# Optimization experiments

Hardware: AMD Instinct MI355X
Metric: run time of the kernel (lower is better)

## Reference

```python
import jax, jax.numpy as jnp
import numpy as np

R = 16            # grid resolution
WIN = 8           # window size (voxels per side)
NW3 = (R // WIN) ** 3   # number of windows = 8
WS = WIN ** 3           # tokens per window = 512
N = R ** 3              # active voxels = 4096
C = 512; H = 8; DH = C // H; L = 8; LAT = 8
NG = 4; VOX = 0.015625; OUTC = 14 * NG; MLP = 4 * C


def _radical_inverse(base, i):
    f = 1.0; r = 0.0
    while i > 0:
        f /= base; r += f * (i % base); i //= base
    return r


def _offset_perturbation():
    # hammersley_sequence(3, i, NG) = [i/NG, phi_2(i), phi_3(i)]
    p = np.array([[i / NG, _radical_inverse(2, i), _radical_inverse(3, i)] for i in range(NG)], np.float32)
    p = p * 2.0 - 1.0
    p = np.clip(p / VOX, -0.99, 0.99)
    return jnp.asarray(np.arctanh(p).astype(np.float32))  # [NG, 3]


def setup_inputs() -> dict:
    key = jax.random.key(0)
    ks = jax.random.split(key, 12)
    nw = R // WIN
    # window-major voxel ordering: dense 16^3 grid grouped into 8^3 windows
    win = np.stack(np.meshgrid(*[np.arange(nw)] * 3, indexing='ij'), -1).reshape(-1, 3)
    inner = np.stack(np.meshgrid(*[np.arange(WIN)] * 3, indexing='ij'), -1).reshape(-1, 3)
    xyz = (win[:, None, :] * WIN + inner[None, :, :]).reshape(-1, 3).astype(np.int32)
    coords = jnp.asarray(np.concatenate([np.zeros((N, 1), np.int32), xyz], axis=1))  # [N,4] (batch,x,y,z)
    s = 0.02
    return {
        'feats': jax.random.normal(ks[0], (N, LAT), jnp.float32),
        'coords': coords,
        'emb_x': jax.random.normal(ks[1], (1024, C // 3), jnp.float32) * s,
        'emb_y': jax.random.normal(ks[2], (1024, C // 3), jnp.float32) * s,
        'emb_z': jax.random.normal(ks[3], (1024, C - 2 * (C // 3)), jnp.float32) * s,
        'w_in': jax.random.normal(ks[4], (LAT, C), jnp.float32) * s,
        'b_in': jnp.zeros((C,), jnp.float32),
        'ln1_g': jnp.ones((L, C), jnp.float32), 'ln1_b': jnp.zeros((L, C), jnp.float32),
        'w_qkv': jax.random.normal(ks[5], (L, C, 3 * C), jnp.float32) * s,
        'b_qkv': jnp.zeros((L, 3 * C), jnp.float32),
        'w_o': jax.random.normal(ks[6], (L, C, C), jnp.float32) * s,
        'b_o': jnp.zeros((L, C), jnp.float32),
        'ln2_g': jnp.ones((L, C), jnp.float32), 'ln2_b': jnp.zeros((L, C), jnp.float32),
        'w_m1': jax.random.normal(ks[7], (L, C, MLP), jnp.float32) * s,
        'b_m1': jnp.zeros((L, MLP), jnp.float32),
        'w_m2': jax.random.normal(ks[8], (L, MLP, C), jnp.float32) * s,
        'b_m2': jnp.zeros((L, C), jnp.float32),
        'w_out': jax.random.normal(ks[9], (C, OUTC), jnp.float32) * s,
        'b_out': jnp.zeros((OUTC,), jnp.float32),
        'offset_perturb': _offset_perturbation(),
    }


def _ln(x, g, b, eps):
    m = jnp.mean(x, axis=-1, keepdims=True)
    v = jnp.var(x, axis=-1, keepdims=True)
    return (x - m) * jax.lax.rsqrt(v + eps) * g + b


def _forward(feats, coords, emb_x, emb_y, emb_z, w_in, b_in, ln1_g, ln1_b,
             w_qkv, b_qkv, w_o, b_o, ln2_g, ln2_b, w_m1, b_m1, w_m2, b_m2,
             w_out, b_out, offset_perturb):
    # input_layer + absolute position embedding (gather from 3 tables)
    h = feats @ w_in + b_in  # [N, C]
    pe = jnp.concatenate([emb_x[coords[:, 1]], emb_y[coords[:, 2]], emb_z[coords[:, 3]]], axis=-1)
    h = h + pe

    def block(h, p):
        l1g, l1b, wq, bq, wo, bo, l2g, l2b, w1, b1, w2, b2 = p
        a = _ln(h, l1g, l1b, 1e-6)
        qkv = (a @ wq + bq).reshape(NW3, WS, 3, H, DH)  # voxels are window-major
        q, k, v = qkv[:, :, 0], qkv[:, :, 1], qkv[:, :, 2]
        scores = jnp.einsum('wqhd,wkhd->whqk', q, k) / jnp.sqrt(jnp.float32(DH))
        attn = jax.nn.softmax(scores, axis=-1)
        o = jnp.einsum('whqk,wkhd->wqhd', attn, v).reshape(N, C)
        h = h + o @ wo + bo
        m = _ln(h, l2g, l2b, 1e-6)
        h = h + jax.nn.gelu(m @ w1 + b1) @ w2 + b2
        return h, None

    params = (ln1_g, ln1_b, w_qkv, b_qkv, w_o, b_o, ln2_g, ln2_b, w_m1, b_m1, w_m2, b_m2)
    h, _ = jax.lax.scan(block, h, params)

    # final non-affine layer_norm + out projection
    h = _ln(h, jnp.ones((C,), h.dtype), jnp.zeros((C,), h.dtype), 1e-5)
    out = h @ w_out + b_out  # [N, 56]

    # to_representation (single batch)
    xyz_base = (coords[:, 1:].astype(jnp.float32) + 0.5) / R  # [N, 3]
    off = out[:, 0:3 * NG].reshape(N, NG, 3) + offset_perturb
    off = jnp.tanh(off) / R * 0.5 * VOX
    _xyz = (xyz_base[:, None, :] + off).reshape(N * NG, 3)
    _fdc = out[:, 3 * NG:6 * NG].reshape(N * NG, 1, 3)
    _scal = out[:, 6 * NG:9 * NG].reshape(N * NG, 3)
    _rot = out[:, 9 * NG:13 * NG].reshape(N * NG, 4)
    _opa = out[:, 13 * NG:14 * NG].reshape(N * NG, 1)
    return _xyz, _fdc, _scal, _rot, _opa


def reference(feats, coords, emb_x, emb_y, emb_z, w_in, b_in, ln1_g, ln1_b,
              w_qkv, b_qkv, w_o, b_o, ln2_g, ln2_b, w_m1, b_m1, w_m2, b_m2,
              w_out, b_out, offset_perturb):
    return _forward(feats, coords, emb_x, emb_y, emb_z, w_in, b_in, ln1_g, ln1_b,
                    w_qkv, b_qkv, w_o, b_o, ln2_g, ln2_b, w_m1, b_m1, w_m2, b_m2,
                    w_out, b_out, offset_perturb)
```

## Files before the change

kernel.cpp:

```cpp
#include <hip/hip_runtime.h>
#include <stdint.h>

typedef unsigned short u16;
typedef short bf16x8 __attribute__((ext_vector_type(8)));
typedef float f32x4 __attribute__((ext_vector_type(4)));

#define NTOK 4096
#define CDIM 512
#define NHEAD 8
#define LAYERS 8
#define MLPD 2048
#define QKVD 1536

__device__ __forceinline__ u16 f2bf(float f){
  union { float f; unsigned u; } c; c.f = f;
  return (u16)((c.u + 0x7FFFu + ((c.u >> 16) & 1u)) >> 16);
}

__device__ __forceinline__ unsigned pack2(float a, float b){
  return (unsigned)f2bf(a) | ((unsigned)f2bf(b) << 16);
}

__device__ __forceinline__ void llds16(const void* g, void* l){
  __builtin_amdgcn_global_load_lds((const __attribute__((address_space(1))) void*)g,
                                   (__attribute__((address_space(3))) void*)l, 16, 0, 0);
}

template<int N> __device__ __forceinline__ void wait_vmcnt(){
  if constexpr (N == 0) asm volatile("s_waitcnt vmcnt(0)" ::: "memory");
  else if constexpr (N == 2) asm volatile("s_waitcnt vmcnt(2)" ::: "memory");
  else if constexpr (N == 4) asm volatile("s_waitcnt vmcnt(4)" ::: "memory");
  else static_assert(N == 0 || N == 2 || N == 4, "unsupported vmcnt");
}

__global__ void kt_transpose(const float* __restrict__ W, u16* __restrict__ Wt, int K, int N){
  __shared__ float tile[32][33];
  int l = blockIdx.z;
  W  += (size_t)l * K * N;
  Wt += (size_t)l * K * N;
  int k0 = blockIdx.y * 32, n0 = blockIdx.x * 32;
  int t = threadIdx.x;
  int r = t >> 3, c4 = (t & 7) << 2;
  float4 v = *(const float4*)&W[(size_t)(k0 + r) * N + n0 + c4];
  tile[r][c4 + 0] = v.x; tile[r][c4 + 1] = v.y; tile[r][c4 + 2] = v.z; tile[r][c4 + 3] = v.w;
  __syncthreads();
  ushort4 o;
  o.x = f2bf(tile[c4 + 0][r]);
  o.y = f2bf(tile[c4 + 1][r]);
  o.z = f2bf(tile[c4 + 2][r]);
  o.w = f2bf(tile[c4 + 3][r]);
  *(ushort4*)&Wt[(size_t)(n0 + r) * K + k0 + c4] = o;
}

__global__ void kt_embed(const float* __restrict__ feats, const int* __restrict__ coords,
                         const float* __restrict__ ex, const float* __restrict__ ey,
                         const float* __restrict__ ez, const float* __restrict__ w_in,
                         const float* __restrict__ b_in, float* __restrict__ h){
  __shared__ float fs[8];
  __shared__ int cc[3];
  int n = blockIdx.x, t = threadIdx.x;
  if (t < 8) fs[t] = feats[n * 8 + t];
  if (t == 8) { cc[0] = coords[n*4+1]; cc[1] = coords[n*4+2]; cc[2] = coords[n*4+3]; }
  __syncthreads();
  for (int c = t; c < CDIM; c += 256){
    float acc = b_in[c];
    #pragma unroll
    for (int i = 0; i < 8; i++) acc += fs[i] * w_in[i * CDIM + c];
    float pe;
    if (c < 170)      pe = ex[cc[0] * 170 + c];
    else if (c < 340) pe = ey[cc[1] * 170 + (c - 170)];
    else              pe = ez[cc[2] * 172 + (c - 340)];
    h[(size_t)n * CDIM + c] = acc + pe;
  }
}

__global__ void kt_ln(const float* __restrict__ h, const float* __restrict__ g,
                      const float* __restrict__ b, u16* __restrict__ out, float eps){
  int wave = threadIdx.x >> 6, lane = threadIdx.x & 63;
  int row = blockIdx.x * 4 + wave;
  const float* hr = h + (size_t)row * CDIM + lane * 8;
  float4 v0 = *(const float4*)hr, v1 = *(const float4*)(hr + 4);
  float x[8] = {v0.x, v0.y, v0.z, v0.w, v1.x, v1.y, v1.z, v1.w};
  float s = 0.f, q = 0.f;
  #pragma unroll
  for (int i = 0; i < 8; i++){ s += x[i]; q += x[i] * x[i]; }
  #pragma unroll
  for (int off = 32; off; off >>= 1){ s += __shfl_xor(s, off); q += __shfl_xor(q, off); }
  float mean = s * (1.0f / CDIM);
  float var  = q * (1.0f / CDIM) - mean * mean;
  float rr = rsqrtf(var + eps);
  int cb = lane * 8;
  u16 u[8];
  #pragma unroll
  for (int i = 0; i < 8; i++)
    u[i] = f2bf((x[i] - mean) * rr * g[cb + i] + b[cb + i]);
  uint4 pk;
  pk.x = (unsigned)u[0] | ((unsigned)u[1] << 16);
  pk.y = (unsigned)u[2] | ((unsigned)u[3] << 16);
  pk.z = (unsigned)u[4] | ((unsigned)u[5] << 16);
  pk.w = (unsigned)u[6] | ((unsigned)u[7] << 16);
  *(uint4*)&out[(size_t)row * CDIM + cb] = pk;
}

template<int BM, int BN, int MODE>
__global__ __launch_bounds__(256) void kt_gemm(
    const u16* __restrict__ A, const u16* __restrict__ Wt, const float* __restrict__ bias,
    u16* __restrict__ outb, float* __restrict__ hres, u16* __restrict__ vT, int N, int K)
{
  constexpr int MF = BM / 32;
  constexpr int NF = BN / 32;
  constexpr int Mt = NTOK / BM;
  constexpr int Mx = Mt / 8;
  __shared__ __align__(16) u16 As[2][BM * 64];
  __shared__ __align__(16) u16 Bs[2][BN * 64];
  int tid = threadIdx.x, wave = tid >> 6, lane = tid & 63;

  int Nt = N / BN;
  int bid = blockIdx.x;
  int xcd = bid & 7, slot = bid >> 3;
  int miL = slot / Nt;
  int ni = slot - miL * Nt;
  int m0 = (xcd * Mx + miL) * BM, n0 = ni * BN;

  int wm = wave >> 1, wn = wave & 1;
  f32x4 acc[MF][NF];
  const f32x4 fzero = {0.f, 0.f, 0.f, 0.f};
  #pragma unroll
  for (int m = 0; m < MF; m++)
    #pragma unroll
    for (int n = 0; n < NF; n++) acc[m][n] = fzero;

  int srow = lane >> 3;
  int sblk = (lane & 7) ^ srow;
  const u16* gA = A  + (size_t)(m0 + wave * 8 + srow) * K + sblk * 8;
  const u16* gB = Wt + (size_t)(n0 + wave * 8 + srow) * K + sblk * 8;

  auto stage = [&](int buf, int kt){
    #pragma unroll
    for (int j = 0; j < MF; j++)
      llds16(gA + (size_t)(j * 32) * K + kt, &As[buf][(j * 32 + wave * 8) * 64]);
    #pragma unroll
    for (int j = 0; j < NF; j++)
      llds16(gB + (size_t)(j * 32) * K + kt, &Bs[buf][(j * 32 + wave * 8) * 64]);
  };

  int nk = K >> 6;
  stage(0, 0);
  __syncthreads();
  int rl = lane & 15, hg = lane >> 4;
  for (int t = 0; t < nk; ++t){
    int cur = t & 1;
    if (t + 1 < nk) stage(cur ^ 1, (t + 1) << 6);
    #pragma unroll
    for (int kk = 0; kk < 2; kk++){
      bf16x8 af[MF], bfr[NF];
      int bl = (kk << 2) + hg;
      #pragma unroll
      for (int m = 0; m < MF; m++){
        int row = wm * (BM / 2) + m * 16 + rl;
        af[m] = *(const bf16x8*)&As[cur][row * 64 + ((bl ^ (row & 7)) << 3)];
      }
      #pragma unroll
      for (int n = 0; n < NF; n++){
        int row = wn * (BN / 2) + n * 16 + rl;
        bfr[n] = *(const bf16x8*)&Bs[cur][row * 64 + ((bl ^ (row & 7)) << 3)];
      }
      #pragma unroll
      for (int m = 0; m < MF; m++)
        #pragma unroll
        for (int n = 0; n < NF; n++)
          acc[m][n] = __builtin_amdgcn_mfma_f32_16x16x32_bf16(af[m], bfr[n], acc[m][n], 0, 0, 0);
    }
    __syncthreads();
  }

  int cl = lane & 15, rg = lane >> 4;
  #pragma unroll
  for (int m = 0; m < MF; m++){
    int row0 = m0 + wm * (BM / 2) + m * 16 + rg * 4;
    #pragma unroll
    for (int n = 0; n < NF; n++){
      int col = n0 + wn * (BN / 2) + n * 16 + cl;
      float bb = bias[col];
      if (MODE == 1){
        #pragma unroll
        for (int r = 0; r < 4; r++){
          size_t idx = (size_t)(row0 + r) * N + col;
          hres[idx] += acc[m][n][r] + bb;
        }
      } else if (MODE == 2){
        #pragma unroll
        for (int r = 0; r < 4; r++){
          float x = acc[m][n][r] + bb;
          float t = 0.7978845608028654f * (x + 0.044715f * x * x * x);
          float sg = 1.0f / (1.0f + __expf(-2.0f * t));
          outb[(size_t)(row0 + r) * N + col] = f2bf(x * sg);
        }
      } else {
        if (col < 1024){
          #pragma unroll
          for (int r = 0; r < 4; r++)
            outb[(size_t)(row0 + r) * N + col] = f2bf(acc[m][n][r] + bb);
        } else {
          int dh = col - 1024;
          int win = row0 >> 9, tin = row0 & 511;
          ushort4 p;
          p.x = f2bf(acc[m][n][0] + bb);
          p.y = f2bf(acc[m][n][1] + bb);
          p.z = f2bf(acc[m][n][2] + bb);
          p.w = f2bf(acc[m][n][3] + bb);
          *(ushort4*)&vT[(size_t)(win * 512 + dh) * 512 + tin] = p;
        }
      }
    }
  }
}

__global__ __launch_bounds__(256) void kt_attn(const u16* __restrict__ qkv,
                                               const u16* __restrict__ vT,
                                               u16* __restrict__ o){
  __shared__ __align__(16) u16 Ks[3][32 * 64];
  __shared__ __align__(16) u16 Vs[3][64 * 32];
  int tid = threadIdx.x, wave = tid >> 6, lane = tid & 63;
  int bx = blockIdx.x;
  int win = bx >> 6, head = (bx >> 3) & 7, q8 = bx & 7;
  int rl = lane & 15, hg = lane >> 4;
  int qbase = win * 512 + q8 * 64 + wave * 16;
  const u16* qptr  = qkv + (size_t)(qbase + rl) * QKVD + head * 64;
  const u16* kbase = qkv + (size_t)(win * 512) * QKVD + 512 + head * 64;
  const u16* vbase = vT + (size_t)(win * 512 + head * 64) * 512;

  int krow = tid >> 3;
  const u16* gK = kbase + (size_t)krow * QKVD + (((tid & 7) ^ (krow & 7)) << 3);
  int vrow = tid >> 2;
  const u16* gV = vbase + (size_t)vrow * 512 + (((tid & 3) ^ (vrow & 3)) << 3);

  auto stage = [&](int buf, int kt){
    llds16(gK + (size_t)kt * QKVD, &Ks[buf][tid * 8]);
    llds16(gV + kt, &Vs[buf][tid * 8]);
  };

  bf16x8 qf0 = *(const bf16x8*)(qptr + hg * 8);
  bf16x8 qf1 = *(const bf16x8*)(qptr + 32 + hg * 8);

  const f32x4 fzero = {0.f, 0.f, 0.f, 0.f};
  f32x4 Oa[4] = {fzero, fzero, fzero, fzero};
  float mrun = -1e30f, lrun = 0.f;

  stage(0, 0);
  stage(1, 32);
  for (int t = 0; t < 16; ++t){
    int cur = t % 3;
    if (t + 1 < 16) wait_vmcnt<2>(); else wait_vmcnt<0>();
    __builtin_amdgcn_s_barrier();
    asm volatile("" ::: "memory");
    if (t + 2 < 16) stage((t + 2) % 3, (t + 2) * 32);

    bf16x8 kf[2][2];
    #pragma unroll
    for (int c = 0; c < 2; c++)
      #pragma unroll
      for (int dk = 0; dk < 2; dk++){
        int row = c * 16 + rl;
        kf[c][dk] = *(const bf16x8*)&Ks[cur][row * 64 + ((((dk << 2) + hg) ^ (rl & 7)) << 3)];
      }
    bf16x8 vf[4];
    #pragma unroll
    for (int d = 0; d < 4; d++){
      int row = d * 16 + rl;
      vf[d] = *(const bf16x8*)&Vs[cur][row * 32 + ((hg ^ (rl & 3)) << 3)];
    }

    f32x4 s0 = fzero, s1 = fzero;
    s0 = __builtin_amdgcn_mfma_f32_16x16x32_bf16(kf[0][0], qf0, s0, 0, 0, 0);
    s0 = __builtin_amdgcn_mfma_f32_16x16x32_bf16(kf[0][1], qf1, s0, 0, 0, 0);
    s1 = __builtin_amdgcn_mfma_f32_16x16x32_bf16(kf[1][0], qf0, s1, 0, 0, 0);
    s1 = __builtin_amdgcn_mfma_f32_16x16x32_bf16(kf[1][1], qf1, s1, 0, 0, 0);
    float v[8];
    #pragma unroll
    for (int r = 0; r < 4; r++){ v[r] = s0[r] * 0.125f; v[4 + r] = s1[r] * 0.125f; }
    float tmax = v[0];
    #pragma unroll
    for (int i = 1; i < 8; i++) tmax = fmaxf(tmax, v[i]);
    tmax = fmaxf(tmax, __shfl_xor(tmax, 16));
    tmax = fmaxf(tmax, __shfl_xor(tmax, 32));
    float mnew = fmaxf(mrun, tmax);
    float corr = __expf(mrun - mnew);
    mrun = mnew;
    float p[8], ps = 0.f;
    #pragma unroll
    for (int i = 0; i < 8; i++){ p[i] = __expf(v[i] - mnew); ps += p[i]; }
    ps += __shfl_xor(ps, 16);
    ps += __shfl_xor(ps, 32);
    lrun = lrun * corr + ps;
    float c0 = __shfl(corr, (hg << 2) + 0);
    float c1 = __shfl(corr, (hg << 2) + 1);
    float c2 = __shfl(corr, (hg << 2) + 2);
    float c3 = __shfl(corr, (hg << 2) + 3);
    #pragma unroll
    for (int d = 0; d < 4; d++){
      Oa[d][0] *= c0; Oa[d][1] *= c1; Oa[d][2] *= c2; Oa[d][3] *= c3;
    }
    unsigned pk00 = pack2(p[0], p[1]);
    unsigned pk01 = pack2(p[2], p[3]);
    unsigned pk10 = pack2(p[4], p[5]);
    unsigned pk11 = pack2(p[6], p[7]);
    int idx0 = rl | ((( hg << 1)      & 3) << 4);
    int idx1 = rl | ((((hg << 1) + 1) & 3) << 4);
    bool hiC = hg >= 2;
    unsigned W0a = __shfl(pk00, idx0), W0b = __shfl(pk10, idx0);
    unsigned W1a = __shfl(pk01, idx0), W1b = __shfl(pk11, idx0);
    unsigned W2a = __shfl(pk00, idx1), W2b = __shfl(pk10, idx1);
    unsigned W3a = __shfl(pk01, idx1), W3b = __shfl(pk11, idx1);
    uint4 W;
    W.x = hiC ? W0b : W0a;
    W.y = hiC ? W1b : W1a;
    W.z = hiC ? W2b : W2a;
    W.w = hiC ? W3b : W3a;
    bf16x8 pf;
    __builtin_memcpy(&pf, &W, 16);
    #pragma unroll
    for (int d = 0; d < 4; d++)
      Oa[d] = __builtin_amdgcn_mfma_f32_16x16x32_bf16(pf, vf[d], Oa[d], 0, 0, 0);
  }

  float l0 = __shfl(lrun, (hg << 2) + 0);
  float l1 = __shfl(lrun, (hg << 2) + 1);
  float l2 = __shfl(lrun, (hg << 2) + 2);
  float l3 = __shfl(lrun, (hg << 2) + 3);
  float li[4] = {1.f / l0, 1.f / l1, 1.f / l2, 1.f / l3};
  #pragma unroll
  for (int d = 0; d < 4; d++)
    #pragma unroll
    for (int r = 0; r < 4; r++){
      int row = qbase + (hg << 2) + r;
      o[(size_t)row * CDIM + head * 64 + d * 16 + rl] = f2bf(Oa[d][r] * li[r]);
    }
}

__global__ void kt_final(const float* __restrict__ h, const float* __restrict__ w_out,
                         const float* __restrict__ b_out, const int* __restrict__ coords,
                         const float* __restrict__ offp, float* __restrict__ out){
  __shared__ float lnv[CDIM];
  __shared__ float ov[56];
  int n = blockIdx.x, lane = threadIdx.x;
  const float* hr = h + (size_t)n * CDIM + lane * 8;
  float4 v0 = *(const float4*)hr, v1 = *(const float4*)(hr + 4);
  float x[8] = {v0.x, v0.y, v0.z, v0.w, v1.x, v1.y, v1.z, v1.w};
  float s = 0.f, q = 0.f;
  #pragma unroll
  for (int i = 0; i < 8; i++){ s += x[i]; q += x[i] * x[i]; }
  #pragma unroll
  for (int off = 32; off; off >>= 1){ s += __shfl_xor(s, off); q += __shfl_xor(q, off); }
  float mean = s * (1.0f / CDIM);
  float var  = q * (1.0f / CDIM) - mean * mean;
  float rr = rsqrtf(var + 1e-5f);
  #pragma unroll
  for (int i = 0; i < 8; i++) lnv[lane * 8 + i] = (x[i] - mean) * rr;
  __syncthreads();
  if (lane < 56){
    float a = b_out[lane];
    for (int k = 0; k < CDIM; k++) a += lnv[k] * w_out[k * 56 + lane];
    ov[lane] = a;
  }
  __syncthreads();
  if (lane < 12){
    int g = lane / 3, d = lane - g * 3;
    float base = ((float)coords[n * 4 + 1 + d] + 0.5f) * (1.0f / 16.0f);
    float t = tanhf(ov[lane] + offp[lane]);
    out[(size_t)n * 12 + lane] = base + t * 4.8828125e-4f;
    out[49152  + (size_t)n * 12 + lane] = ov[12 + lane];
    out[98304  + (size_t)n * 12 + lane] = ov[24 + lane];
  }
  if (lane < 16) out[147456 + (size_t)n * 16 + lane] = ov[36 + lane];
  if (lane < 4)  out[212992 + (size_t)n * 4  + lane] = ov[52 + lane];
}

extern "C" void kernel_launch(void* const* d_in, const int* in_sizes, int n_in,
                              void* d_out, int out_size, void* d_ws, size_t ws_size,
                              hipStream_t stream) {
  const float* feats = (const float*)d_in[0];
  const int*   coords = (const int*)d_in[1];
  const float* emb_x = (const float*)d_in[2];
  const float* emb_y = (const float*)d_in[3];
  const float* emb_z = (const float*)d_in[4];
  const float* w_in  = (const float*)d_in[5];
  const float* b_in  = (const float*)d_in[6];
  const float* ln1_g = (const float*)d_in[7];
  const float* ln1_b = (const float*)d_in[8];
  const float* w_qkv = (const float*)d_in[9];
  const float* b_qkv = (const float*)d_in[10];
  const float* w_o   = (const float*)d_in[11];
  const float* b_o   = (const float*)d_in[12];
  const float* ln2_g = (const float*)d_in[13];
  const float* ln2_b = (const float*)d_in[14];
  const float* w_m1  = (const float*)d_in[15];
  const float* b_m1  = (const float*)d_in[16];
  const float* w_m2  = (const float*)d_in[17];
  const float* b_m2  = (const float*)d_in[18];
  const float* w_out = (const float*)d_in[19];
  const float* b_out = (const float*)d_in[20];
  const float* offp  = (const float*)d_in[21];

  char* ws = (char*)d_ws;
  auto carve = [&](size_t bytes){ char* p = ws; ws += (bytes + 255) & ~(size_t)255; return p; };
  float* h   = (float*)carve((size_t)NTOK * CDIM * 4);
  u16* a     = (u16*)carve((size_t)NTOK * CDIM * 2);
  u16* qkvb  = (u16*)carve((size_t)NTOK * QKVD * 2);
  u16* vT    = (u16*)carve((size_t)NTOK * CDIM * 2);
  u16* ob    = (u16*)carve((size_t)NTOK * CDIM * 2);
  u16* ub    = (u16*)carve((size_t)NTOK * MLPD * 2);
  u16* wqkvT = (u16*)carve((size_t)LAYERS * QKVD * CDIM * 2);
  u16* woT   = (u16*)carve((size_t)LAYERS * CDIM * CDIM * 2);
  u16* wm1T  = (u16*)carve((size_t)LAYERS * MLPD * CDIM * 2);
  u16* wm2T  = (u16*)carve((size_t)LAYERS * CDIM * MLPD * 2);

  kt_transpose<<<dim3(QKVD/32, CDIM/32, LAYERS), 256, 0, stream>>>(w_qkv, wqkvT, CDIM, QKVD);
  kt_transpose<<<dim3(CDIM/32, CDIM/32, LAYERS), 256, 0, stream>>>(w_o,   woT,   CDIM, CDIM);
  kt_transpose<<<dim3(MLPD/32, CDIM/32, LAYERS), 256, 0, stream>>>(w_m1,  wm1T,  CDIM, MLPD);
  kt_transpose<<<dim3(CDIM/32, MLPD/32, LAYERS), 256, 0, stream>>>(w_m2,  wm2T,  MLPD, CDIM);
  kt_embed<<<NTOK, 256, 0, stream>>>(feats, coords, emb_x, emb_y, emb_z, w_in, b_in, h);

  for (int l = 0; l < LAYERS; ++l){
    kt_ln<<<NTOK/4, 256, 0, stream>>>(h, ln1_g + l*CDIM, ln1_b + l*CDIM, a, 1e-6f);
    kt_gemm<128,128,0><<<(NTOK/128)*(QKVD/128), 256, 0, stream>>>(
        a, wqkvT + (size_t)l*QKVD*CDIM, b_qkv + l*QKVD, qkvb, nullptr, vT, QKVD, CDIM);
    kt_attn<<<512, 256, 0, stream>>>(qkvb, vT, ob);
    kt_gemm<64,64,1><<<(NTOK/64)*(CDIM/64), 256, 0, stream>>>(
        ob, woT + (size_t)l*CDIM*CDIM, b_o + l*CDIM, nullptr, h, nullptr, CDIM, CDIM);
    kt_ln<<<NTOK/4, 256, 0, stream>>>(h, ln2_g + l*CDIM, ln2_b + l*CDIM, a, 1e-6f);
    kt_gemm<128,128,2><<<(NTOK/128)*(MLPD/128), 256, 0, stream>>>(
        a, wm1T + (size_t)l*MLPD*CDIM, b_m1 + l*MLPD, ub, nullptr, nullptr, MLPD, CDIM);
    kt_gemm<64,64,1><<<(NTOK/64)*(CDIM/64), 256, 0, stream>>>(
        ub, wm2T + (size_t)l*CDIM*MLPD, b_m2 + l*CDIM, nullptr, h, nullptr, CDIM, MLPD);
  }
  kt_final<<<NTOK, 64, 0, stream>>>(h, w_out, b_out, coords, offp, (float*)d_out);
}
```

Baseline: 855.2 us.

## Fuse LayerNorm into QKV and MLP1 GEMM A-operand loading

Removes the standalone LayerNorm kernels and instead has the QKV and MLP-up GEMMs read fp32 residual rows directly. Each block first computes per-row mean and rstd into shared memory, then normalizes, converts to bf16 and writes swizzled A tiles into LDS in register-staged double buffering. This drops two launches per layer and the bf16 activation round trip through global memory. In exchange, every N-tile block recomputes row statistics and reads fp32 A (twice the bytes of bf16), which is redundant work across the 12 or 16 column tiles.

```diff
diff --git a/kernel.cpp b/kernel.cpp
--- a/kernel.cpp
+++ b/kernel.cpp
@@ -74,37 +74,11 @@
   }
 }
 
-__global__ void kt_ln(const float* __restrict__ h, const float* __restrict__ g,
-                      const float* __restrict__ b, u16* __restrict__ out, float eps){
-  int wave = threadIdx.x >> 6, lane = threadIdx.x & 63;
-  int row = blockIdx.x * 4 + wave;
-  const float* hr = h + (size_t)row * CDIM + lane * 8;
-  float4 v0 = *(const float4*)hr, v1 = *(const float4*)(hr + 4);
-  float x[8] = {v0.x, v0.y, v0.z, v0.w, v1.x, v1.y, v1.z, v1.w};
-  float s = 0.f, q = 0.f;
-  #pragma unroll
-  for (int i = 0; i < 8; i++){ s += x[i]; q += x[i] * x[i]; }
-  #pragma unroll
-  for (int off = 32; off; off >>= 1){ s += __shfl_xor(s, off); q += __shfl_xor(q, off); }
-  float mean = s * (1.0f / CDIM);
-  float var  = q * (1.0f / CDIM) - mean * mean;
-  float rr = rsqrtf(var + eps);
-  int cb = lane * 8;
-  u16 u[8];
-  #pragma unroll
-  for (int i = 0; i < 8; i++)
-    u[i] = f2bf((x[i] - mean) * rr * g[cb + i] + b[cb + i]);
-  uint4 pk;
-  pk.x = (unsigned)u[0] | ((unsigned)u[1] << 16);
-  pk.y = (unsigned)u[2] | ((unsigned)u[3] << 16);
-  pk.z = (unsigned)u[4] | ((unsigned)u[5] << 16);
-  pk.w = (unsigned)u[6] | ((unsigned)u[7] << 16);
-  *(uint4*)&out[(size_t)row * CDIM + cb] = pk;
-}
-
-template<int BM, int BN, int MODE>
+template<int BM, int BN, int MODE, bool LNA>
 __global__ __launch_bounds__(256) void kt_gemm(
-    const u16* __restrict__ A, const u16* __restrict__ Wt, const float* __restrict__ bias,
+    const u16* __restrict__ A, const float* __restrict__ hA,
+    const float* __restrict__ lng, const float* __restrict__ lnb,
+    const u16* __restrict__ Wt, const float* __restrict__ bias,
     u16* __restrict__ outb, float* __restrict__ hres, u16* __restrict__ vT, int N, int K)
 {
   constexpr int MF = BM / 32;
@@ -113,6 +87,11 @@
   constexpr int Mx = Mt / 8;
   __shared__ __align__(16) u16 As[2][BM * 64];
   __shared__ __align__(16) u16 Bs[2][BN * 64];
+  __shared__ float Gs[LNA ? CDIM : 1];
+  __shared__ float Bt[LNA ? CDIM : 1];
+  __shared__ float Mu[LNA ? BM : 1];
+  __shared__ float Rs[LNA ? BM : 1];
+
   int tid = threadIdx.x, wave = tid >> 6, lane = tid & 63;
 
   int Nt = N / BN;
@@ -135,22 +114,95 @@
   const u16* gA = A  + (size_t)(m0 + wave * 8 + srow) * K + sblk * 8;
   const u16* gB = Wt + (size_t)(n0 + wave * 8 + srow) * K + sblk * 8;
 
-  auto stage = [&](int buf, int kt){
-    #pragma unroll
-    for (int j = 0; j < MF; j++)
-      llds16(gA + (size_t)(j * 32) * K + kt, &As[buf][(j * 32 + wave * 8) * 64]);
+  auto stageB = [&](int buf, int kt){
     #pragma unroll
     for (int j = 0; j < NF; j++)
       llds16(gB + (size_t)(j * 32) * K + kt, &Bs[buf][(j * 32 + wave * 8) * 64]);
   };
+  auto stageA = [&](int buf, int kt){
+    #pragma unroll
+    for (int j = 0; j < MF; j++)
+      llds16(gA + (size_t)(j * 32) * K + kt, &As[buf][(j * 32 + wave * 8) * 64]);
+  };
+
+  int r8 = tid >> 3, cb = tid & 7;
+  float mu_[MF], rs_[MF];
+
+  if constexpr (LNA){
+    if (tid < 128)      *(float4*)&Gs[tid * 4] = *(const float4*)&lng[tid * 4];
+    else                *(float4*)&Bt[(tid - 128) * 4] = *(const float4*)&lnb[(tid - 128) * 4];
+    int half = lane >> 5, l32 = lane & 31;
+    for (int rr = 0; rr < 16; ++rr){
+      int rloc = wave * 32 + rr * 2 + half;
+      const float4* hp = (const float4*)(hA + (size_t)(m0 + rloc) * CDIM + l32 * 16);
+      float4 a0 = hp[0], a1 = hp[1], a2 = hp[2], a3 = hp[3];
+      float x[16] = {a0.x,a0.y,a0.z,a0.w, a1.x,a1.y,a1.z,a1.w,
+                     a2.x,a2.y,a2.z,a2.w, a3.x,a3.y,a3.z,a3.w};
+      float s = 0.f, q = 0.f;
+      #pragma unroll
+      for (int i = 0; i < 16; i++){ s += x[i]; q += x[i] * x[i]; }
+      #pragma unroll
+      for (int off = 1; off < 32; off <<= 1){ s += __shfl_xor(s, off); q += __shfl_xor(q, off); }
+      if (l32 == 0){
+        float mean = s * (1.0f / CDIM);
+        float var  = q * (1.0f / CDIM) - mean * mean;
+        Mu[rloc] = mean;
+        Rs[rloc] = rsqrtf(var + 1e-6f);
+      }
+    }
+    __syncthreads();
+    #pragma unroll
+    for (int j = 0; j < MF; j++){ mu_[j] = Mu[j * 32 + r8]; rs_[j] = Rs[j * 32 + r8]; }
+  }
+
+  auto loadA = [&](int kt, float4* r0, float4* r1){
+    #pragma unroll
+    for (int j = 0; j < MF; j++){
+      const float* hp = hA + (size_t)(m0 + j * 32 + r8) * CDIM + kt + cb * 8;
+      r0[j] = *(const float4*)hp;
+      r1[j] = *(const float4*)(hp + 4);
+    }
+  };
+  auto writeA = [&](int buf, int kt, const float4* r0, const float4* r1){
+    #pragma unroll
+    for (int j = 0; j < MF; j++){
+      float x[8] = {r0[j].x, r0[j].y, r0[j].z, r0[j].w,
+                    r1[j].x, r1[j].y, r1[j].z, r1[j].w};
+      int cbase = kt + cb * 8;
+      u16 w[8];
+      #pragma unroll
+      for (int i = 0; i < 8; i++)
+        w[i] = f2bf((x[i] - mu_[j]) * rs_[j] * Gs[cbase + i] + Bt[cbase + i]);
+      uint4 pk;
+      pk.x = (unsigned)w[0] | ((unsigned)w[1] << 16);
+      pk.y = (unsigned)w[2] | ((unsigned)w[3] << 16);
+      pk.z = (unsigned)w[4] | ((unsigned)w[5] << 16);
+      pk.w = (unsigned)w[6] | ((unsigned)w[7] << 16);
+      *(uint4*)&As[buf][(j * 32 + r8) * 64 + ((cb ^ (r8 & 7)) << 3)] = pk;
+    }
+  };
 
   int nk = K >> 6;
-  stage(0, 0);
+  int rl = lane & 15, hg = lane >> 4;
+
+  stageB(0, 0);
+  if constexpr (LNA){
+    float4 r0[MF], r1[MF];
+    loadA(0, r0, r1);
+    writeA(0, 0, r0, r1);
+  } else {
+    stageA(0, 0);
+  }
   __syncthreads();
-  int rl = lane & 15, hg = lane >> 4;
+
   for (int t = 0; t < nk; ++t){
     int cur = t & 1;
-    if (t + 1 < nk) stage(cur ^ 1, (t + 1) << 6);
+    float4 r0[MF], r1[MF];
+    if (t + 1 < nk){
+      stageB(cur ^ 1, (t + 1) << 6);
+      if constexpr (LNA) loadA((t + 1) << 6, r0, r1);
+      else               stageA(cur ^ 1, (t + 1) << 6);
+    }
     #pragma unroll
     for (int kk = 0; kk < 2; kk++){
       bf16x8 af[MF], bfr[NF];
@@ -170,6 +222,9 @@
         #pragma unroll
         for (int n = 0; n < NF; n++)
           acc[m][n] = __builtin_amdgcn_mfma_f32_16x16x32_bf16(af[m], bfr[n], acc[m][n], 0, 0, 0);
+    }
+    if constexpr (LNA){
+      if (t + 1 < nk) writeA(cur ^ 1, (t + 1) << 6, r0, r1);
     }
     __syncthreads();
   }
@@ -405,7 +460,6 @@
   char* ws = (char*)d_ws;
   auto carve = [&](size_t bytes){ char* p = ws; ws += (bytes + 255) & ~(size_t)255; return p; };
   float* h   = (float*)carve((size_t)NTOK * CDIM * 4);
-  u16* a     = (u16*)carve((size_t)NTOK * CDIM * 2);
   u16* qkvb  = (u16*)carve((size_t)NTOK * QKVD * 2);
   u16* vT    = (u16*)carve((size_t)NTOK * CDIM * 2);
   u16* ob    = (u16*)carve((size_t)NTOK * CDIM * 2);
@@ -422,17 +476,19 @@
   kt_embed<<<NTOK, 256, 0, stream>>>(feats, coords, emb_x, emb_y, emb_z, w_in, b_in, h);
 
   for (int l = 0; l < LAYERS; ++l){
-    kt_ln<<<NTOK/4, 256, 0, stream>>>(h, ln1_g + l*CDIM, ln1_b + l*CDIM, a, 1e-6f);
-    kt_gemm<128,128,0><<<(NTOK/128)*(QKVD/128), 256, 0, stream>>>(
-        a, wqkvT + (size_t)l*QKVD*CDIM, b_qkv + l*QKVD, qkvb, nullptr, vT, QKVD, CDIM);
+    kt_gemm<128,128,0,true><<<(NTOK/128)*(QKVD/128), 256, 0, stream>>>(
+        nullptr, h, ln1_g + l*CDIM, ln1_b + l*CDIM,
+        wqkvT + (size_t)l*QKVD*CDIM, b_qkv + l*QKVD, qkvb, nullptr, vT, QKVD, CDIM);
     kt_attn<<<512, 256, 0, stream>>>(qkvb, vT, ob);
-    kt_gemm<64,64,1><<<(NTOK/64)*(CDIM/64), 256, 0, stream>>>(
-        ob, woT + (size_t)l*CDIM*CDIM, b_o + l*CDIM, nullptr, h, nullptr, CDIM, CDIM);
-    kt_ln<<<NTOK/4, 256, 0, stream>>>(h, ln2_g + l*CDIM, ln2_b + l*CDIM, a, 1e-6f);
-    kt_gemm<128,128,2><<<(NTOK/128)*(MLPD/128), 256, 0, stream>>>(
-        a, wm1T + (size_t)l*MLPD*CDIM, b_m1 + l*MLPD, ub, nullptr, nullptr, MLPD, CDIM);
-    kt_gemm<64,64,1><<<(NTOK/64)*(CDIM/64), 256, 0, stream>>>(
-        ub, wm2T + (size_t)l*CDIM*MLPD, b_m2 + l*CDIM, nullptr, h, nullptr, CDIM, MLPD);
+    kt_gemm<64,64,1,false><<<(NTOK/64)*(CDIM/64), 256, 0, stream>>>(
+        ob, nullptr, nullptr, nullptr,
+        woT + (size_t)l*CDIM*CDIM, b_o + l*CDIM, nullptr, h, nullptr, CDIM, CDIM);
+    kt_gemm<128,128,2,true><<<(NTOK/128)*(MLPD/128), 256, 0, stream>>>(
+        nullptr, h, ln2_g + l*CDIM, ln2_b + l*CDIM,
+        wm1T + (size_t)l*MLPD*CDIM, b_m1 + l*MLPD, ub, nullptr, nullptr, MLPD, CDIM);
+    kt_gemm<64,64,1,false><<<(NTOK/64)*(CDIM/64), 256, 0, stream>>>(
+        ub, nullptr, nullptr, nullptr,
+        wm2T + (size_t)l*CDIM*MLPD, b_m2 + l*CDIM, nullptr, h, nullptr, CDIM, MLPD);
   }
   kt_final<<<NTOK, 64, 0, stream>>>(h, w_out, b_out, coords, offp, (float*)d_out);
 }
```

Measured after the change: 1.057 ms. +23.6%, slower.

## Rewrite final LN+projection as tiled MFMA GEMM and merge weight transposes

Applied to the files above, without the earlier changes.

The final layernorm and output projection now run as a 64-row-tile bf16 MFMA GEMM, with LN fused into A-tile staging and w_out pre-transposed and zero-padded to 64 columns. This replaces the old per-token scalar dot-product kernel. The four weight-transpose launches, plus the new w_out transpose, are merged into one launch to cut launch overhead. The final projection now uses bf16 inputs instead of fp32, which lowers precision, and it launches only 64 blocks.

```diff
diff --git a/kernel.cpp b/kernel.cpp
--- a/kernel.cpp
+++ b/kernel.cpp
@@ -33,16 +33,49 @@
   else static_assert(N == 0 || N == 2 || N == 4, "unsupported vmcnt");
 }
 
-__global__ void kt_transpose(const float* __restrict__ W, u16* __restrict__ Wt, int K, int N){
+__global__ void kt_transpose_all(const float* __restrict__ wqkv, const float* __restrict__ wo,
+                                 const float* __restrict__ wm1, const float* __restrict__ wm2,
+                                 const float* __restrict__ wout,
+                                 u16* __restrict__ qkvT, u16* __restrict__ oT,
+                                 u16* __restrict__ m1T, u16* __restrict__ m2T,
+                                 u16* __restrict__ outT){
   __shared__ float tile[32][33];
-  int l = blockIdx.z;
-  W  += (size_t)l * K * N;
-  Wt += (size_t)l * K * N;
-  int k0 = blockIdx.y * 32, n0 = blockIdx.x * 32;
+  int bid = blockIdx.x;
+  const float* W; u16* Wt; int K, N, k0, n0; bool guard = false;
+  if (bid < 6144){
+    int l = bid / 768, r = bid % 768;
+    W = wqkv + (size_t)l * 512 * 1536; Wt = qkvT + (size_t)l * 512 * 1536;
+    K = 512; N = 1536; n0 = (r % 48) * 32; k0 = (r / 48) * 32;
+  } else if (bid < 8192){
+    int b = bid - 6144; int l = b / 256, r = b % 256;
+    W = wo + (size_t)l * 512 * 512; Wt = oT + (size_t)l * 512 * 512;
+    K = 512; N = 512; n0 = (r % 16) * 32; k0 = (r / 16) * 32;
+  } else if (bid < 16384){
+    int b = bid - 8192; int l = b / 1024, r = b % 1024;
+    W = wm1 + (size_t)l * 512 * 2048; Wt = m1T + (size_t)l * 512 * 2048;
+    K = 512; N = 2048; n0 = (r % 64) * 32; k0 = (r / 64) * 32;
+  } else if (bid < 24576){
+    int b = bid - 16384; int l = b / 1024, r = b % 1024;
+    W = wm2 + (size_t)l * 2048 * 512; Wt = m2T + (size_t)l * 2048 * 512;
+    K = 2048; N = 512; n0 = (r % 16) * 32; k0 = (r / 16) * 32;
+  } else {
+    int r = bid - 24576;
+    W = wout; Wt = outT;
+    K = 512; N = 56; n0 = (r % 2) * 32; k0 = (r / 2) * 32;
+    guard = true;
+  }
   int t = threadIdx.x;
   int r = t >> 3, c4 = (t & 7) << 2;
-  float4 v = *(const float4*)&W[(size_t)(k0 + r) * N + n0 + c4];
-  tile[r][c4 + 0] = v.x; tile[r][c4 + 1] = v.y; tile[r][c4 + 2] = v.z; tile[r][c4 + 3] = v.w;
+  if (guard){
+    #pragma unroll
+    for (int i = 0; i < 4; i++){
+      int col = n0 + c4 + i;
+      tile[r][c4 + i] = (col < N) ? W[(size_t)(k0 + r) * N + col] : 0.f;
+    }
+  } else {
+    float4 v = *(const float4*)&W[(size_t)(k0 + r) * N + n0 + c4];
+    tile[r][c4 + 0] = v.x; tile[r][c4 + 1] = v.y; tile[r][c4 + 2] = v.z; tile[r][c4 + 3] = v.w;
+  }
   __syncthreads();
   ushort4 o;
   o.x = f2bf(tile[c4 + 0][r]);
@@ -338,42 +371,141 @@
     }
 }
 
-__global__ void kt_final(const float* __restrict__ h, const float* __restrict__ w_out,
-                         const float* __restrict__ b_out, const int* __restrict__ coords,
-                         const float* __restrict__ offp, float* __restrict__ out){
-  __shared__ float lnv[CDIM];
-  __shared__ float ov[56];
-  int n = blockIdx.x, lane = threadIdx.x;
-  const float* hr = h + (size_t)n * CDIM + lane * 8;
-  float4 v0 = *(const float4*)hr, v1 = *(const float4*)(hr + 4);
-  float x[8] = {v0.x, v0.y, v0.z, v0.w, v1.x, v1.y, v1.z, v1.w};
-  float s = 0.f, q = 0.f;
-  #pragma unroll
-  for (int i = 0; i < 8; i++){ s += x[i]; q += x[i] * x[i]; }
-  #pragma unroll
-  for (int off = 32; off; off >>= 1){ s += __shfl_xor(s, off); q += __shfl_xor(q, off); }
-  float mean = s * (1.0f / CDIM);
-  float var  = q * (1.0f / CDIM) - mean * mean;
-  float rr = rsqrtf(var + 1e-5f);
-  #pragma unroll
-  for (int i = 0; i < 8; i++) lnv[lane * 8 + i] = (x[i] - mean) * rr;
+__global__ __launch_bounds__(256) void kt_final(const float* __restrict__ h,
+                                                const u16* __restrict__ WoT,
+                                                const float* __restrict__ b_out,
+                                                const int* __restrict__ coords,
+                                                const float* __restrict__ offp,
+                                                float* __restrict__ out){
+  __shared__ __align__(16) u16 As[2][64 * 64];
+  __shared__ __align__(16) u16 Bs[2][64 * 64];
+  __shared__ float Mu[64], Rs[64];
+  int tid = threadIdx.x, wave = tid >> 6, lane = tid & 63;
+  int m0 = blockIdx.x * 64;
+  int wm = wave >> 1, wn = wave & 1;
+
+  for (int rr = 0; rr < 16; ++rr){
+    int rloc = wave * 16 + rr;
+    const float* hp = h + (size_t)(m0 + rloc) * CDIM + lane * 8;
+    float4 v0 = *(const float4*)hp, v1 = *(const float4*)(hp + 4);
+    float x[8] = {v0.x, v0.y, v0.z, v0.w, v1.x, v1.y, v1.z, v1.w};
+    float s = 0.f, q = 0.f;
+    #pragma unroll
+    for (int i = 0; i < 8; i++){ s += x[i]; q += x[i] * x[i]; }
+    #pragma unroll
+    for (int off = 32; off; off >>= 1){ s += __shfl_xor(s, off); q += __shfl_xor(q, off); }
+    if (lane == 0){
+      float mean = s * (1.0f / CDIM);
+      float var  = q * (1.0f / CDIM) - mean * mean;
+      Mu[rloc] = mean;
+      Rs[rloc] = rsqrtf(var + 1e-5f);
+    }
+  }
   __syncthreads();
-  if (lane < 56){
-    float a = b_out[lane];
-    for (int k = 0; k < CDIM; k++) a += lnv[k] * w_out[k * 56 + lane];
-    ov[lane] = a;
-  }
+
+  int ar = tid >> 2, ac = tid & 3;
+  float mu_ = Mu[ar], rs_ = Rs[ar];
+
+  auto stageA = [&](int buf, int kt){
+    const float* hp = h + (size_t)(m0 + ar) * CDIM + kt + ac * 16;
+    float4 a0 = *(const float4*)hp, a1 = *(const float4*)(hp + 4);
+    float4 a2 = *(const float4*)(hp + 8), a3 = *(const float4*)(hp + 12);
+    float x[16] = {a0.x,a0.y,a0.z,a0.w, a1.x,a1.y,a1.z,a1.w,
+                   a2.x,a2.y,a2.z,a2.w, a3.x,a3.y,a3.z,a3.w};
+    u16 w[16];
+    #pragma unroll
+    for (int i = 0; i < 16; i++) w[i] = f2bf((x[i] - mu_) * rs_);
+    uint4 p0, p1;
+    p0.x = (unsigned)w[0] | ((unsigned)w[1] << 16);
+    p0.y = (unsigned)w[2] | ((unsigned)w[3] << 16);
+    p0.z = (unsigned)w[4] | ((unsigned)w[5] << 16);
+    p0.w = (unsigned)w[6] | ((unsigned)w[7] << 16);
+    p1.x = (unsigned)w[8] | ((unsigned)w[9] << 16);
+    p1.y = (unsigned)w[10] | ((unsigned)w[11] << 16);
+    p1.z = (unsigned)w[12] | ((unsigned)w[13] << 16);
+    p1.w = (unsigned)w[14] | ((unsigned)w[15] << 16);
+    int j0 = ac * 2, j1 = ac * 2 + 1;
+    *(uint4*)&As[buf][ar * 64 + ((j0 ^ (ar & 7)) << 3)] = p0;
+    *(uint4*)&As[buf][ar * 64 + ((j1 ^ (ar & 7)) << 3)] = p1;
+  };
+
+  int srow = lane >> 3;
+  int sblk = (lane & 7) ^ srow;
+  const u16* gB = WoT + (size_t)(wave * 8 + srow) * CDIM + sblk * 8;
+  auto stageB = [&](int buf, int kt){
+    #pragma unroll
+    for (int j = 0; j < 2; j++)
+      llds16(gB + (size_t)(j * 32) * CDIM + kt, &Bs[buf][(j * 32 + wave * 8) * 64]);
+  };
+
+  f32x4 acc[2][2];
+  const f32x4 fzero = {0.f, 0.f, 0.f, 0.f};
+  acc[0][0] = fzero; acc[0][1] = fzero; acc[1][0] = fzero; acc[1][1] = fzero;
+
+  stageB(0, 0);
+  stageA(0, 0);
   __syncthreads();
-  if (lane < 12){
-    int g = lane / 3, d = lane - g * 3;
-    float base = ((float)coords[n * 4 + 1 + d] + 0.5f) * (1.0f / 16.0f);
-    float t = tanhf(ov[lane] + offp[lane]);
-    out[(size_t)n * 12 + lane] = base + t * 4.8828125e-4f;
-    out[49152  + (size_t)n * 12 + lane] = ov[12 + lane];
-    out[98304  + (size_t)n * 12 + lane] = ov[24 + lane];
-  }
-  if (lane < 16) out[147456 + (size_t)n * 16 + lane] = ov[36 + lane];
-  if (lane < 4)  out[212992 + (size_t)n * 4  + lane] = ov[52 + lane];
+  int rl = lane & 15, hg = lane >> 4;
+  for (int t = 0; t < 8; ++t){
+    int cur = t & 1;
+    if (t + 1 < 8){
+      stageB(cur ^ 1, (t + 1) << 6);
+      stageA(cur ^ 1, (t + 1) << 6);
+    }
+    #pragma unroll
+    for (int kk = 0; kk < 2; kk++){
+      bf16x8 af[2], bfr[2];
+      int bl = (kk << 2) + hg;
+      #pragma unroll
+      for (int m = 0; m < 2; m++){
+        int row = wm * 32 + m * 16 + rl;
+        af[m] = *(const bf16x8*)&As[cur][row * 64 + ((bl ^ (row & 7)) << 3)];
+      }
+      #pragma unroll
+      for (int n = 0; n < 2; n++){
+        int row = wn * 32 + n * 16 + rl;
+        bfr[n] = *(const bf16x8*)&Bs[cur][row * 64 + ((bl ^ (row & 7)) << 3)];
+      }
+      #pragma unroll
+      for (int m = 0; m < 2; m++)
+        #pragma unroll
+        for (int n = 0; n < 2; n++)
+          acc[m][n] = __builtin_amdgcn_mfma_f32_16x16x32_bf16(af[m], bfr[n], acc[m][n], 0, 0, 0);
+    }
+    __syncthreads();
+  }
+
+  int cl = lane & 15, rg = lane >> 4;
+  #pragma unroll
+  for (int m = 0; m < 2; m++){
+    int row0 = m0 + wm * 32 + m * 16 + rg * 4;
+    #pragma unroll
+    for (int n = 0; n < 2; n++){
+      int col = wn * 32 + n * 16 + cl;
+      if (col < 56){
+        float bb = b_out[col];
+        #pragma unroll
+        for (int r = 0; r < 4; r++){
+          int row = row0 + r;
+          float v = acc[m][n][r] + bb;
+          if (col < 12){
+            int d = col - (col / 3) * 3;
+            float base = ((float)coords[row * 4 + 1 + d] + 0.5f) * (1.0f / 16.0f);
+            float tt = tanhf(v + offp[col]);
+            out[(size_t)row * 12 + col] = base + tt * 4.8828125e-4f;
+          } else if (col < 24){
+            out[49152 + (size_t)row * 12 + (col - 12)] = v;
+          } else if (col < 36){
+            out[98304 + (size_t)row * 12 + (col - 24)] = v;
+          } else if (col < 52){
+            out[147456 + (size_t)row * 16 + (col - 36)] = v;
+          } else {
+            out[212992 + (size_t)row * 4 + (col - 52)] = v;
+          }
+        }
+      }
+    }
+  }
 }
 
 extern "C" void kernel_launch(void* const* d_in, const int* in_sizes, int n_in,
@@ -414,11 +546,10 @@
   u16* woT   = (u16*)carve((size_t)LAYERS * CDIM * CDIM * 2);
   u16* wm1T  = (u16*)carve((size_t)LAYERS * MLPD * CDIM * 2);
   u16* wm2T  = (u16*)carve((size_t)LAYERS * CDIM * MLPD * 2);
-
-  kt_transpose<<<dim3(QKVD/32, CDIM/32, LAYERS), 256, 0, stream>>>(w_qkv, wqkvT, CDIM, QKVD);
-  kt_transpose<<<dim3(CDIM/32, CDIM/32, LAYERS), 256, 0, stream>>>(w_o,   woT,   CDIM, CDIM);
-  kt_transpose<<<dim3(MLPD/32, CDIM/32, LAYERS), 256, 0, stream>>>(w_m1,  wm1T,  CDIM, MLPD);
-  kt_transpose<<<dim3(CDIM/32, MLPD/32, LAYERS), 256, 0, stream>>>(w_m2,  wm2T,  MLPD, CDIM);
+  u16* woutT = (u16*)carve((size_t)64 * CDIM * 2);
+
+  kt_transpose_all<<<24608, 256, 0, stream>>>(w_qkv, w_o, w_m1, w_m2, w_out,
+                                              wqkvT, woT, wm1T, wm2T, woutT);
   kt_embed<<<NTOK, 256, 0, stream>>>(feats, coords, emb_x, emb_y, emb_z, w_in, b_in, h);
 
   for (int l = 0; l < LAYERS; ++l){
@@ -434,5 +565,5 @@
     kt_gemm<64,64,1><<<(NTOK/64)*(CDIM/64), 256, 0, stream>>>(
         ub, wm2T + (size_t)l*CDIM*MLPD, b_m2 + l*CDIM, nullptr, h, nullptr, CDIM, MLPD);
   }
-  kt_final<<<NTOK, 64, 0, stream>>>(h, w_out, b_out, coords, offp, (float*)d_out);
-}
+  kt_final<<<64, 256, 0, stream>>>(h, woutT, b_out, coords, offp, (float*)d_out);
+}
```

New measurement: 848.4 us. Within noise of the previous version (-0.8%).
